# Kernel tuning notes

Hardware: AMD Instinct MI355X
Metric: run time of the kernel (lower is better)

## Reference

```python
import jax, jax.numpy as jnp
import numpy as np
import math

DIM = 512
HEADS = 8          # dim // num_head_channels = 512 // 64
HEAD_CH = 64
GROUPS = 32        # guided-diffusion normalization() = GroupNorm(32, dim)
EPS = 1e-5
CROSS_DIM = 768


def setup_inputs() -> dict:
    key = jax.random.key(0)
    ks = jax.random.split(key, 8)
    B, C, Hs, Ws, L = 16, DIM, 32, 32, 77
    x = jax.random.normal(ks[0], (B, C, Hs, Ws), dtype=jnp.float32)
    c = jax.random.normal(ks[1], (B, CROSS_DIM, L), dtype=jnp.float32)
    # GroupNorm affine params
    gamma = jnp.ones((C,), jnp.float32)
    beta = jnp.zeros((C,), jnp.float32)
    # 1x1 conv weights stored as [out, in]
    w_qkv = jax.random.normal(ks[2], (3 * C, C), jnp.float32) / math.sqrt(C)
    b_qkv = jnp.zeros((3 * C,), jnp.float32)
    w_c = jax.random.normal(ks[3], (2 * C, CROSS_DIM), jnp.float32) / math.sqrt(CROSS_DIM)
    b_c = jnp.zeros((2 * C,), jnp.float32)
    # NOTE: original proj_out is zero-initialized (zero_module); we use small
    # random weights so the reference exercises non-trivial math end-to-end.
    w_p = jax.random.normal(ks[4], (C, C), jnp.float32) / math.sqrt(C)
    b_p = jnp.zeros((C,), jnp.float32)
    return {"x": x, "c": c, "gamma": gamma, "beta": beta,
            "w_qkv": w_qkv, "b_qkv": b_qkv, "w_c": w_c, "b_c": b_c,
            "w_p": w_p, "b_p": b_p}


def reference(x, c, gamma, beta, w_qkv, b_qkv, w_c, b_c, w_p, b_p):
    B, C, Hs, Ws = x.shape
    T = Hs * Ws
    xf = x.reshape(B, C, T)

    # GroupNorm(32) over (channels_per_group, spatial)
    xg = xf.reshape(B, GROUPS, C // GROUPS, T)
    mean = xg.mean(axis=(2, 3), keepdims=True)
    var = xg.var(axis=(2, 3), keepdims=True)
    xn = ((xg - mean) * jax.lax.rsqrt(var + EPS)).reshape(B, C, T)
    xn = xn * gamma[None, :, None] + beta[None, :, None]

    # qkv 1x1 conv: [B, 3C, T]
    qkv = jnp.einsum('oc,bct->bot', w_qkv, xn) + b_qkv[None, :, None]
    q, k, v = jnp.split(qkv, 3, axis=1)
    q = q.reshape(B, HEADS, HEAD_CH, T)
    k = k.reshape(B, HEADS, HEAD_CH, T)
    v = v.reshape(B, HEADS, HEAD_CH, T)

    # cross-attn cond kv: [B, 2C, L] -> concat on sequence axis
    ckv = jnp.einsum('oc,bcl->bol', w_c, c) + b_c[None, :, None]
    kc, vc = jnp.split(ckv, 2, axis=1)
    L = c.shape[-1]
    k = jnp.concatenate([k, kc.reshape(B, HEADS, HEAD_CH, L)], axis=-1)
    v = jnp.concatenate([v, vc.reshape(B, HEADS, HEAD_CH, L)], axis=-1)

    scale = 1.0 / math.sqrt(HEAD_CH)
    # scores [B, H, T, T+L]; scale applied inside softmax as in FusedSoftmaxMaybeApex
    logits = jnp.einsum('bhct,bhcs->bhts', q, k) * scale
    w = jax.nn.softmax(logits, axis=-1)
    a = jnp.einsum('bhts,bhcs->bhct', w, v).reshape(B, C, T)

    h = jnp.einsum('oc,bct->bot', w_p, a) + b_p[None, :, None]
    return (xf + h).reshape(B, C, Hs, Ws)
```

## Files before the change

### kernel.cpp

```cpp
#include <hip/hip_runtime.h>

#define B_   16
#define C_   512
#define T_   1024
#define H_   8
#define D_   64
#define G_   32
#define L_   77
#define S_   1101
#define SPAD 1152
#define NPAD 51
#define CD_  768
#define BT_  (B_*T_)
#define SROW 72
#define QSC  0.18033688011112042f

typedef __bf16 bf16x8 __attribute__((ext_vector_type(8)));
typedef float  f32x4  __attribute__((ext_vector_type(4)));

static __device__ __forceinline__ unsigned short f2bf(float f) {
    unsigned int u = __float_as_uint(f);
    u = (u + 0x7fffu + ((u >> 16) & 1u)) >> 16;
    return (unsigned short)u;
}

static __device__ __forceinline__ unsigned int pk_bf16(float a, float b) {
    unsigned int d;
    asm("v_cvt_pk_bf16_f32 %0, %1, %2" : "=v"(d) : "v"(a), "v"(b));
    return d;
}

static __device__ __forceinline__ void gload_lds16(const unsigned short* g,
                                                   unsigned short* l) {
    __builtin_amdgcn_global_load_lds(
        (const __attribute__((address_space(1))) unsigned int*)g,
        (__attribute__((address_space(3))) unsigned int*)l, 16, 0, 0);
}

__global__ __launch_bounds__(256) void prep_k(const float* __restrict__ x,
                                              float* __restrict__ stats,
                                              const float* __restrict__ w_qkv,
                                              const float* __restrict__ w_p,
                                              const float* __restrict__ w_c,
                                              const float* __restrict__ cin,
                                              unsigned short* __restrict__ wqkv_pk,
                                              unsigned short* __restrict__ wp_pk,
                                              unsigned short* __restrict__ wc_pk,
                                              unsigned short* __restrict__ cpk) {
    const int tid = threadIdx.x;
    if (blockIdx.x < 512) {
        const int bg = blockIdx.x;
        const float* p = x + (size_t)bg * 16384;
        float s = 0.f, s2 = 0.f;
        for (int i = tid; i < 16384; i += 256) {
            float v = p[i];
            s += v; s2 += v * v;
        }
        __shared__ float rs[256], rs2[256];
        rs[tid] = s; rs2[tid] = s2;
        __syncthreads();
        for (int off = 128; off > 0; off >>= 1) {
            if (tid < off) { rs[tid] += rs[tid + off]; rs2[tid] += rs2[tid + off]; }
            __syncthreads();
        }
        if (tid == 0) {
            float mean = rs[0] * (1.0f / 16384.0f);
            float var  = rs2[0] * (1.0f / 16384.0f) - mean * mean;
            stats[2 * bg]     = mean;
            stats[2 * bg + 1] = rsqrtf(var + 1e-5f);
        }
        return;
    }
    if (blockIdx.x < 1408) {
        const int cid = (blockIdx.x - 512) * 256 + tid;
        const float* src;
        unsigned short* dst;
        if (cid < 98304) {
            const int ml = cid & 127, k8 = (cid >> 7) & 7, kt = (cid >> 10) & 7, mt = cid >> 13;
            src = w_qkv + (size_t)(mt * 128 + ml) * 512 + kt * 64 + k8 * 8;
            dst = wqkv_pk + (size_t)cid * 8;
        } else if (cid < 131072) {
            const int c2 = cid - 98304;
            const int ml = c2 & 127, k8 = (c2 >> 7) & 7, kt = (c2 >> 10) & 7, mt = c2 >> 13;
            src = w_p + (size_t)(mt * 128 + ml) * 512 + kt * 64 + k8 * 8;
            dst = wp_pk + (size_t)c2 * 8;
        } else {
            const int c3 = cid - 131072;
            const int ml = c3 & 127, k8 = (c3 >> 7) & 7;
            const int ktmt = c3 >> 10;
            const int kt = ktmt % 12, mt = ktmt / 12;
            src = w_c + (size_t)(mt * 128 + ml) * 768 + kt * 64 + k8 * 8;
            dst = wc_pk + (size_t)c3 * 8;
        }
        const float4 v0 = *(const float4*)src, v1 = *(const float4*)(src + 4);
        unsigned short tmp[8];
        tmp[0] = f2bf(v0.x); tmp[1] = f2bf(v0.y); tmp[2] = f2bf(v0.z); tmp[3] = f2bf(v0.w);
        tmp[4] = f2bf(v1.x); tmp[5] = f2bf(v1.y); tmp[6] = f2bf(v1.z); tmp[7] = f2bf(v1.w);
        *(uint4*)dst = *(uint4*)tmp;
        return;
    }
    const int idx2 = blockIdx.x - 1408;
    const int kt = idx2 % 12, b = idx2 / 12;
#pragma unroll
    for (int it = 0; it < 4; it++) {
        const int idx = it * 256 + tid;
        const int k8 = idx >> 7, l = idx & 127;
        unsigned short tmp[8];
        const float* src = cin + ((size_t)b * CD_ + kt * 64 + k8 * 8) * L_ + l;
#pragma unroll
        for (int q = 0; q < 8; q++)
            tmp[q] = (l < L_) ? f2bf(src[(size_t)q * L_]) : (unsigned short)0;
        *(uint4*)&cpk[(size_t)b * 98304 + ((size_t)(kt * 8 + k8)) * 1024 + (size_t)l * 8] =
            *(uint4*)tmp;
    }
}

__global__ __launch_bounds__(256) void gn_apply_t(const float* __restrict__ x,
                                                  const float* __restrict__ stats,
                                                  const float* __restrict__ gamma,
                                                  const float* __restrict__ beta,
                                                  unsigned short* __restrict__ xnT) {
    const int t0 = blockIdx.x * 64, kt = blockIdx.y, b = blockIdx.z;
    const int c0 = kt * 64;
    const int tid = threadIdx.x;
    __shared__ float st[64][66];
#pragma unroll
    for (int it = 0; it < 4; it++) {
        const int fid = it * 256 + tid;
        const int ci = fid >> 4, t4 = (fid & 15) * 4;
        const int c = c0 + ci;
        const float4 xv = *(const float4*)&x[((size_t)(b * C_ + c) << 10) + t0 + t4];
        const int bg = b * G_ + (c >> 4);
        const float mean = stats[2 * bg], istd = stats[2 * bg + 1];
        const float gs = gamma[c] * istd, gb = beta[c] - mean * gs;
        st[t4 + 0][ci] = xv.x * gs + gb;
        st[t4 + 1][ci] = xv.y * gs + gb;
        st[t4 + 2][ci] = xv.z * gs + gb;
        st[t4 + 3][ci] = xv.w * gs + gb;
    }
    __syncthreads();
#pragma unroll
    for (int it = 0; it < 2; it++) {
        const int cid = it * 256 + tid;
        const int k8 = cid >> 6, tl = cid & 63;
        const int n = (b << 10) + t0 + tl;
        const int nt = n >> 7, nm = n & 127;
        unsigned short tmp[8];
        const float* src = &st[tl][k8 * 8];
#pragma unroll
        for (int q = 0; q < 8; q++) tmp[q] = f2bf(src[q]);
        *(uint4*)&xnT[(((size_t)nt * 8 + kt) * 8 + k8) * 1024 + (size_t)nm * 8] = *(uint4*)tmp;
    }
}

template<int MODE, int KT>
__global__ __launch_bounds__(256) void mgemm_k(const unsigned short* __restrict__ Apk,
                                               const unsigned short* __restrict__ Bpk,
                                               const float* __restrict__ bias,
                                               const float* __restrict__ resid,
                                               unsigned short* __restrict__ qpk,
                                               unsigned short* __restrict__ kpk,
                                               unsigned short* __restrict__ vpk,
                                               float* __restrict__ outp) {
    __shared__ unsigned short lds[18432];
    const int tid = threadIdx.x, wave = tid >> 6, lane = tid & 63;
    const int quad = lane >> 4, l16 = lane & 15;
    const int nt = blockIdx.x, mt = blockIdx.y;
    const int mw = (wave & 1) * 64, nw = (wave >> 1) * 64;

    f32x4 acc[4][4];
#pragma unroll
    for (int i = 0; i < 4; i++)
#pragma unroll
        for (int j = 0; j < 4; j++) acc[i][j] = (f32x4){0.f, 0.f, 0.f, 0.f};

    const unsigned short* Ab = Apk + (size_t)mt * KT * 8192;
    const unsigned short* Bb = Bpk + ((MODE == 2) ? (size_t)blockIdx.z * KT * 8192 : 0)
                                   + (size_t)nt * KT * 8192;

    for (int kt = 0; kt < KT; kt++) {
        const unsigned short* as = Ab + kt * 8192 + wave * 2048 + lane * 8;
        const unsigned short* bs = Bb + kt * 8192 + wave * 2048 + lane * 8;
        unsigned short* la = lds + wave * 2048;
        unsigned short* lb = lds + 8192 + wave * 2048;
#pragma unroll
        for (int j = 0; j < 4; j++) {
            gload_lds16(as + j * 512, la + j * 512);
            gload_lds16(bs + j * 512, lb + j * 512);
        }
        __syncthreads();
#pragma unroll
        for (int kh = 0; kh < 2; kh++) {
            const int k8 = kh * 4 + quad;
            bf16x8 af[4], bfr[4];
#pragma unroll
            for (int i = 0; i < 4; i++) {
                af[i]  = *(const bf16x8*)&lds[(size_t)(k8 * 128 + mw + i * 16 + l16) * 8];
                bfr[i] = *(const bf16x8*)&lds[8192 + (size_t)(k8 * 128 + nw + i * 16 + l16) * 8];
            }
#pragma unroll
            for (int mi = 0; mi < 4; mi++)
#pragma unroll
                for (int ni = 0; ni < 4; ni++)
                    acc[mi][ni] = __builtin_amdgcn_mfma_f32_16x16x32_bf16(
                        af[mi], bfr[ni], acc[mi][ni], 0, 0, 0);
        }
        __syncthreads();
    }

    const int gm0 = mt * 128 + mw;
    const int gn0 = nt * 128 + nw;

    if (MODE == 1) {
        const int b = gn0 >> 10, t0 = gn0 & 1023;
#pragma unroll
        for (int mi = 0; mi < 4; mi++) {
#pragma unroll
            for (int r = 0; r < 4; r++) {
                const int m = gm0 + mi * 16 + quad * 4 + r;
                const float bv = bias[m];
                const size_t rowb = ((size_t)(b * C_ + m) << 10) + t0;
#pragma unroll
                for (int ni = 0; ni < 4; ni++) {
                    const size_t a = rowb + ni * 16 + l16;
                    outp[a] = acc[mi][ni][r] + bv + resid[a];
                }
            }
        }
        return;
    }

    const int region = gm0 >> 9;
    const int h = (gm0 & 511) >> 6;
    const int b = (MODE == 2) ? blockIdx.z : (gn0 >> 10);
    const int bh = b * 8 + h;
    const bool vregion = (MODE == 0) ? (region == 2) : (region == 1);

    if (!vregion) {
        const float sc = (MODE == 0 && region == 0) ? QSC : 1.0f;
        unsigned short* base;
        int trow0;
        size_t tilestride;
        if (MODE == 0) {
            base = (region == 0) ? qpk + (size_t)bh * 16 * 4096
                                 : kpk + (size_t)bh * 18 * 4096;
            trow0 = gn0 & 1023;
        } else {
            base = kpk + (size_t)(bh * 18 + 16 + (gn0 >> 6)) * 4096;
            trow0 = -1;
        }
        (void)tilestride;
#pragma unroll
        for (int mi = 0; mi < 4; mi++) {
            const int k8 = mi * 2 + (quad >> 1);
            const int sub = (quad & 1) * 4;
#pragma unroll
            for (int ni = 0; ni < 4; ni++) {
                float vv[4];
                bool valid = true;
                if (MODE == 2) valid = (gn0 + ni * 16 + l16) < L_;
#pragma unroll
                for (int r = 0; r < 4; r++)
                    vv[r] = valid ? (acc[mi][ni][r] + bias[gm0 + mi * 16 + quad * 4 + r]) * sc
                                  : 0.f;
                uint2 d;
                d.x = pk_bf16(vv[0], vv[1]);
                d.y = pk_bf16(vv[2], vv[3]);
                unsigned short* dst;
                if (MODE == 0) {
                    const int t = trow0 + ni * 16 + l16;
                    dst = base + (size_t)(t >> 6) * 4096 + ((size_t)k8 * 64 + (t & 63)) * 8 + sub;
                } else {
                    const int row = ni * 16 + l16;
                    dst = base + ((size_t)k8 * 64 + row) * 8 + sub;
                }
                *(uint2*)dst = d;
            }
        }
    } else {
        unsigned short* wlds = lds + wave * 4608;
#pragma unroll
        for (int mi = 0; mi < 4; mi++)
#pragma unroll
            for (int ni = 0; ni < 4; ni++) {
                bool valid = true;
                if (MODE == 2) valid = (gn0 + ni * 16 + l16) < L_;
#pragma unroll
                for (int r = 0; r < 4; r++) {
                    const float v = valid ? acc[mi][ni][r] + bias[gm0 + mi * 16 + quad * 4 + r]
                                          : 0.f;
                    wlds[(mi * 16 + quad * 4 + r) * SROW + ni * 16 + l16] = f2bf(v);
                }
            }
        __syncthreads();
        const int stile = (MODE == 0) ? ((gn0 & 1023) >> 6) : (16 + (gn0 >> 6));
        unsigned short* dst = vpk + (size_t)(bh * 18 + stile) * 4096;
        const int sk8 = lane & 7, cb = lane >> 3;
#pragma unroll
        for (int it = 0; it < 8; it++) {
            const int ch = it * 8 + cb;
            *(uint4*)&dst[((size_t)sk8 * 64 + ch) * 8] =
                *(const uint4*)&wlds[ch * SROW + sk8 * 8];
        }
    }
}

__global__ __launch_bounds__(256) void flash_k(const unsigned short* __restrict__ qpk,
                                               const unsigned short* __restrict__ kpk,
                                               const unsigned short* __restrict__ vpk,
                                               unsigned short* __restrict__ aT) {
    __shared__ __align__(16) unsigned short ks[4096];
    __shared__ __align__(16) unsigned short vs[4096];
    __shared__ __align__(16) unsigned short psA[4 * 16 * SROW];

    const int tid  = threadIdx.x;
    const int wave = tid >> 6, lane = tid & 63;
    const int quad = lane >> 4, l16 = lane & 15;
    const int bh  = blockIdx.x;
    const int b = bh >> 3, h = bh & 7;
    const int qt0 = blockIdx.y * 64;

    const unsigned short* qtb = qpk + ((size_t)bh * 16 + blockIdx.y) * 4096;
    const int qrow = wave * 16 + l16;
    const bf16x8 bq0 = *(const bf16x8*)&qtb[((size_t)quad * 64 + qrow) * 8];
    const bf16x8 bq1 = *(const bf16x8*)&qtb[((size_t)(quad + 4) * 64 + qrow) * 8];

    unsigned short* ps = psA + wave * 16 * SROW;

    float rsum = 0.f;
    f32x4 o_acc[4];
#pragma unroll
    for (int nb = 0; nb < 4; nb++) o_acc[nb] = (f32x4){0.f, 0.f, 0.f, 0.f};

    for (int stile = 0; stile < 18; stile++) {
        const unsigned short* kt = kpk + ((size_t)bh * 18 + stile) * 4096 + wave * 1024 + lane * 8;
        const unsigned short* vt = vpk + ((size_t)bh * 18 + stile) * 4096 + wave * 1024 + lane * 8;
        unsigned short* lk = ks + wave * 1024;
        unsigned short* lv = vs + wave * 1024;
        gload_lds16(kt, lk);       gload_lds16(kt + 512, lk + 512);
        gload_lds16(vt, lv);       gload_lds16(vt + 512, lv + 512);
        __syncthreads();

        f32x4 sacc[4];
#pragma unroll
        for (int sb = 0; sb < 4; sb++) {
            const bf16x8 ak0 = *(const bf16x8*)&ks[((size_t)quad * 64 + sb * 16 + l16) * 8];
            const bf16x8 ak1 = *(const bf16x8*)&ks[((size_t)(quad + 4) * 64 + sb * 16 + l16) * 8];
            f32x4 z = (f32x4){0.f, 0.f, 0.f, 0.f};
            z = __builtin_amdgcn_mfma_f32_16x16x32_bf16(ak0, bq0, z, 0, 0, 0);
            z = __builtin_amdgcn_mfma_f32_16x16x32_bf16(ak1, bq1, z, 0, 0, 0);
            sacc[sb] = z;
        }

#pragma unroll
        for (int sb = 0; sb < 4; sb++) {
            const float e0 = __builtin_exp2f(sacc[sb][0]);
            const float e1 = __builtin_exp2f(sacc[sb][1]);
            const float e2 = __builtin_exp2f(sacc[sb][2]);
            const float e3 = __builtin_exp2f(sacc[sb][3]);
            rsum += (e0 + e1) + (e2 + e3);
            uint2 d;
            d.x = pk_bf16(e0, e1);
            d.y = pk_bf16(e2, e3);
            *(uint2*)&ps[l16 * SROW + sb * 16 + quad * 4] = d;
        }
        asm volatile("s_waitcnt lgkmcnt(0)" ::: "memory");

        const bf16x8 ap0 = *(const bf16x8*)&ps[l16 * SROW + quad * 8];
        const bf16x8 ap1 = *(const bf16x8*)&ps[l16 * SROW + 32 + quad * 8];
#pragma unroll
        for (int nb = 0; nb < 4; nb++) {
            const bf16x8 bv0 = *(const bf16x8*)&vs[((size_t)quad * 64 + nb * 16 + l16) * 8];
            const bf16x8 bv1 = *(const bf16x8*)&vs[((size_t)(quad + 4) * 64 + nb * 16 + l16) * 8];
            o_acc[nb] = __builtin_amdgcn_mfma_f32_16x16x32_bf16(ap0, bv0, o_acc[nb], 0, 0, 0);
            o_acc[nb] = __builtin_amdgcn_mfma_f32_16x16x32_bf16(ap1, bv1, o_acc[nb], 0, 0, 0);
        }
        __syncthreads();
    }

    float lsum = rsum;
    lsum += __shfl_xor(lsum, 16);
    lsum += __shfl_xor(lsum, 32);
    float linv[4];
#pragma unroll
    for (int r = 0; r < 4; r++) {
        const float lr = __shfl(lsum, quad * 4 + r);
        linv[r] = 1.0f / (lr - (float)NPAD);
    }

#pragma unroll
    for (int nb = 0; nb < 4; nb++)
#pragma unroll
        for (int r = 0; r < 4; r++)
            ps[(quad * 4 + r) * SROW + nb * 16 + l16] = f2bf(o_acc[nb][r] * linv[r]);
    asm volatile("s_waitcnt lgkmcnt(0)" ::: "memory");
    const int k8 = lane >> 3;
#pragma unroll
    for (int it = 0; it < 2; it++) {
        const int tl = (lane & 7) + it * 8;
        const int n = (b << 10) + qt0 + wave * 16 + tl;
        const int ntb = n >> 7, nm = n & 127;
        *(uint4*)&aT[(((size_t)ntb * 8 + h) * 8 + k8) * 1024 + (size_t)nm * 8] =
            *(const uint4*)&ps[tl * SROW + k8 * 8];
    }
}

extern "C" void kernel_launch(void* const* d_in, const int* in_sizes, int n_in,
                              void* d_out, int out_size, void* d_ws, size_t ws_size,
                              hipStream_t stream) {
    const float* x     = (const float*)d_in[0];
    const float* cin   = (const float*)d_in[1];
    const float* gamma = (const float*)d_in[2];
    const float* beta  = (const float*)d_in[3];
    const float* w_qkv = (const float*)d_in[4];
    const float* b_qkv = (const float*)d_in[5];
    const float* w_c   = (const float*)d_in[6];
    const float* b_c   = (const float*)d_in[7];
    const float* w_p   = (const float*)d_in[8];
    const float* b_p   = (const float*)d_in[9];
    float* out = (float*)d_out;

    float* ws    = (float*)d_ws;
    float* stats = ws;
    unsigned short* xnT     = (unsigned short*)(ws + 1024);
    unsigned short* wqkv_pk = xnT + 8388608;
    unsigned short* wp_pk   = wqkv_pk + 786432;
    unsigned short* wc_pk   = wp_pk + 262144;
    unsigned short* cpk     = wc_pk + 786432;
    unsigned short* qpk     = cpk + 1572864;
    unsigned short* kpk     = qpk + 8388608;
    unsigned short* vpk     = kpk + 9437184;
    unsigned short* aT      = vpk + 9437184;

    prep_k<<<dim3(1600), 256, 0, stream>>>(x, stats, w_qkv, w_p, w_c, cin,
                                           wqkv_pk, wp_pk, wc_pk, cpk);
    gn_apply_t<<<dim3(16, 8, 16), 256, 0, stream>>>(x, stats, gamma, beta, xnT);
    mgemm_k<0, 8><<<dim3(128, 12), 256, 0, stream>>>(wqkv_pk, xnT, b_qkv, nullptr,
                                                     qpk, kpk, vpk, nullptr);
    mgemm_k<2, 12><<<dim3(1, 8, 16), 256, 0, stream>>>(wc_pk, cpk, b_c, nullptr,
                                                       nullptr, kpk, vpk, nullptr);
    flash_k<<<dim3(128, 16), 256, 0, stream>>>(qpk, kpk, vpk, aT);
    mgemm_k<1, 8><<<dim3(128, 4), 256, 0, stream>>>(wp_pk, aT, b_p, x,
                                                    nullptr, nullptr, nullptr, out);
}
```

Measured before the change: 277.2 us.

## Process two query sub-tiles per wave in flash attention to reuse K/V loads

Each wave of the flash attention kernel now handles 32 query rows (two 16-row sub-tiles) instead of 16, so a block covers 128 queries and the grid's y dimension halves. Each K and V tile staged in LDS, and the K/V fragments read from it, now feed twice as many MFMAs, cutting global K/V traffic and barrier count per query. The cost is higher register use, doubled P scratch in LDS and half as many blocks. A launch-bounds hint of 4 waves per SIMD is added to keep occupancy.

Measured after the change: 268.5 us. 3.1% less time.

```diff
diff --git a/kernel.cpp b/kernel.cpp
--- a/kernel.cpp
+++ b/kernel.cpp
@@ -305,32 +305,38 @@
     }
 }
 
-__global__ __launch_bounds__(256) void flash_k(const unsigned short* __restrict__ qpk,
-                                               const unsigned short* __restrict__ kpk,
-                                               const unsigned short* __restrict__ vpk,
-                                               unsigned short* __restrict__ aT) {
+__global__ __launch_bounds__(256, 4) void flash_k(const unsigned short* __restrict__ qpk,
+                                                  const unsigned short* __restrict__ kpk,
+                                                  const unsigned short* __restrict__ vpk,
+                                                  unsigned short* __restrict__ aT) {
     __shared__ __align__(16) unsigned short ks[4096];
     __shared__ __align__(16) unsigned short vs[4096];
-    __shared__ __align__(16) unsigned short psA[4 * 16 * SROW];
+    __shared__ __align__(16) unsigned short psA[4 * 32 * SROW];
 
     const int tid  = threadIdx.x;
     const int wave = tid >> 6, lane = tid & 63;
     const int quad = lane >> 4, l16 = lane & 15;
     const int bh  = blockIdx.x;
     const int b = bh >> 3, h = bh & 7;
-    const int qt0 = blockIdx.y * 64;
-
-    const unsigned short* qtb = qpk + ((size_t)bh * 16 + blockIdx.y) * 4096;
-    const int qrow = wave * 16 + l16;
-    const bf16x8 bq0 = *(const bf16x8*)&qtb[((size_t)quad * 64 + qrow) * 8];
-    const bf16x8 bq1 = *(const bf16x8*)&qtb[((size_t)(quad + 4) * 64 + qrow) * 8];
-
-    unsigned short* ps = psA + wave * 16 * SROW;
-
-    float rsum = 0.f;
-    f32x4 o_acc[4];
-#pragma unroll
-    for (int nb = 0; nb < 4; nb++) o_acc[nb] = (f32x4){0.f, 0.f, 0.f, 0.f};
+    const int qt0 = blockIdx.y * 128;
+
+    const unsigned short* qtb = qpk + ((size_t)bh * 16 + blockIdx.y * 2 + (wave >> 1)) * 4096;
+    const int qr0 = (wave & 1) * 32 + l16;
+    bf16x8 bq0[2], bq1[2];
+#pragma unroll
+    for (int s = 0; s < 2; s++) {
+        bq0[s] = *(const bf16x8*)&qtb[((size_t)quad * 64 + qr0 + s * 16) * 8];
+        bq1[s] = *(const bf16x8*)&qtb[((size_t)(quad + 4) * 64 + qr0 + s * 16) * 8];
+    }
+
+    unsigned short* ps = psA + wave * 32 * SROW;
+
+    float rsum[2] = {0.f, 0.f};
+    f32x4 o_acc[2][4];
+#pragma unroll
+    for (int s = 0; s < 2; s++)
+#pragma unroll
+        for (int nb = 0; nb < 4; nb++) o_acc[s][nb] = (f32x4){0.f, 0.f, 0.f, 0.f};
 
     for (int stile = 0; stile < 18; stile++) {
         const unsigned short* kt = kpk + ((size_t)bh * 18 + stile) * 4096 + wave * 1024 + lane * 8;
@@ -341,64 +347,83 @@
         gload_lds16(vt, lv);       gload_lds16(vt + 512, lv + 512);
         __syncthreads();
 
-        f32x4 sacc[4];
+        f32x4 sacc[2][4];
 #pragma unroll
         for (int sb = 0; sb < 4; sb++) {
             const bf16x8 ak0 = *(const bf16x8*)&ks[((size_t)quad * 64 + sb * 16 + l16) * 8];
             const bf16x8 ak1 = *(const bf16x8*)&ks[((size_t)(quad + 4) * 64 + sb * 16 + l16) * 8];
-            f32x4 z = (f32x4){0.f, 0.f, 0.f, 0.f};
-            z = __builtin_amdgcn_mfma_f32_16x16x32_bf16(ak0, bq0, z, 0, 0, 0);
-            z = __builtin_amdgcn_mfma_f32_16x16x32_bf16(ak1, bq1, z, 0, 0, 0);
-            sacc[sb] = z;
-        }
-
-#pragma unroll
-        for (int sb = 0; sb < 4; sb++) {
-            const float e0 = __builtin_exp2f(sacc[sb][0]);
-            const float e1 = __builtin_exp2f(sacc[sb][1]);
-            const float e2 = __builtin_exp2f(sacc[sb][2]);
-            const float e3 = __builtin_exp2f(sacc[sb][3]);
-            rsum += (e0 + e1) + (e2 + e3);
-            uint2 d;
-            d.x = pk_bf16(e0, e1);
-            d.y = pk_bf16(e2, e3);
-            *(uint2*)&ps[l16 * SROW + sb * 16 + quad * 4] = d;
+#pragma unroll
+            for (int s = 0; s < 2; s++) {
+                f32x4 z = (f32x4){0.f, 0.f, 0.f, 0.f};
+                z = __builtin_amdgcn_mfma_f32_16x16x32_bf16(ak0, bq0[s], z, 0, 0, 0);
+                z = __builtin_amdgcn_mfma_f32_16x16x32_bf16(ak1, bq1[s], z, 0, 0, 0);
+                sacc[s][sb] = z;
+            }
+        }
+
+#pragma unroll
+        for (int s = 0; s < 2; s++) {
+#pragma unroll
+            for (int sb = 0; sb < 4; sb++) {
+                const float e0 = __builtin_exp2f(sacc[s][sb][0]);
+                const float e1 = __builtin_exp2f(sacc[s][sb][1]);
+                const float e2 = __builtin_exp2f(sacc[s][sb][2]);
+                const float e3 = __builtin_exp2f(sacc[s][sb][3]);
+                rsum[s] += (e0 + e1) + (e2 + e3);
+                uint2 d;
+                d.x = pk_bf16(e0, e1);
+                d.y = pk_bf16(e2, e3);
+                *(uint2*)&ps[(s * 16 + l16) * SROW + sb * 16 + quad * 4] = d;
+            }
         }
         asm volatile("s_waitcnt lgkmcnt(0)" ::: "memory");
 
-        const bf16x8 ap0 = *(const bf16x8*)&ps[l16 * SROW + quad * 8];
-        const bf16x8 ap1 = *(const bf16x8*)&ps[l16 * SROW + 32 + quad * 8];
+        bf16x8 ap0[2], ap1[2];
+#pragma unroll
+        for (int s = 0; s < 2; s++) {
+            ap0[s] = *(const bf16x8*)&ps[(s * 16 + l16) * SROW + quad * 8];
+            ap1[s] = *(const bf16x8*)&ps[(s * 16 + l16) * SROW + 32 + quad * 8];
+        }
 #pragma unroll
         for (int nb = 0; nb < 4; nb++) {
             const bf16x8 bv0 = *(const bf16x8*)&vs[((size_t)quad * 64 + nb * 16 + l16) * 8];
             const bf16x8 bv1 = *(const bf16x8*)&vs[((size_t)(quad + 4) * 64 + nb * 16 + l16) * 8];
-            o_acc[nb] = __builtin_amdgcn_mfma_f32_16x16x32_bf16(ap0, bv0, o_acc[nb], 0, 0, 0);
-            o_acc[nb] = __builtin_amdgcn_mfma_f32_16x16x32_bf16(ap1, bv1, o_acc[nb], 0, 0, 0);
-        }
-        __syncthreads();
-    }
-
-    float lsum = rsum;
-    lsum += __shfl_xor(lsum, 16);
-    lsum += __shfl_xor(lsum, 32);
-    float linv[4];
-#pragma unroll
-    for (int r = 0; r < 4; r++) {
-        const float lr = __shfl(lsum, quad * 4 + r);
-        linv[r] = 1.0f / (lr - (float)NPAD);
-    }
-
-#pragma unroll
-    for (int nb = 0; nb < 4; nb++)
-#pragma unroll
-        for (int r = 0; r < 4; r++)
-            ps[(quad * 4 + r) * SROW + nb * 16 + l16] = f2bf(o_acc[nb][r] * linv[r]);
+#pragma unroll
+            for (int s = 0; s < 2; s++) {
+                o_acc[s][nb] = __builtin_amdgcn_mfma_f32_16x16x32_bf16(ap0[s], bv0, o_acc[s][nb], 0, 0, 0);
+                o_acc[s][nb] = __builtin_amdgcn_mfma_f32_16x16x32_bf16(ap1[s], bv1, o_acc[s][nb], 0, 0, 0);
+            }
+        }
+        __syncthreads();
+    }
+
+    float linv[2][4];
+#pragma unroll
+    for (int s = 0; s < 2; s++) {
+        float lsum = rsum[s];
+        lsum += __shfl_xor(lsum, 16);
+        lsum += __shfl_xor(lsum, 32);
+#pragma unroll
+        for (int r = 0; r < 4; r++) {
+            const float lr = __shfl(lsum, quad * 4 + r);
+            linv[s][r] = 1.0f / (lr - (float)NPAD);
+        }
+    }
+
+#pragma unroll
+    for (int s = 0; s < 2; s++)
+#pragma unroll
+        for (int nb = 0; nb < 4; nb++)
+#pragma unroll
+            for (int r = 0; r < 4; r++)
+                ps[(s * 16 + quad * 4 + r) * SROW + nb * 16 + l16] =
+                    f2bf(o_acc[s][nb][r] * linv[s][r]);
     asm volatile("s_waitcnt lgkmcnt(0)" ::: "memory");
     const int k8 = lane >> 3;
 #pragma unroll
-    for (int it = 0; it < 2; it++) {
+    for (int it = 0; it < 4; it++) {
         const int tl = (lane & 7) + it * 8;
-        const int n = (b << 10) + qt0 + wave * 16 + tl;
+        const int n = (b << 10) + qt0 + wave * 32 + tl;
         const int ntb = n >> 7, nm = n & 127;
         *(uint4*)&aT[(((size_t)ntb * 8 + h) * 8 + k8) * 1024 + (size_t)nm * 8] =
             *(const uint4*)&ps[tl * SROW + k8 * 8];
@@ -439,7 +464,7 @@
                                                      qpk, kpk, vpk, nullptr);
     mgemm_k<2, 12><<<dim3(1, 8, 16), 256, 0, stream>>>(wc_pk, cpk, b_c, nullptr,
                                                        nullptr, kpk, vpk, nullptr);
-    flash_k<<<dim3(128, 16), 256, 0, stream>>>(qpk, kpk, vpk, aT);
+    flash_k<<<dim3(128, 8), 256, 0, stream>>>(qpk, kpk, vpk, aT);
     mgemm_k<1, 8><<<dim3(128, 4), 256, 0, stream>>>(wp_pk, aT, b_p, x,
                                                     nullptr, nullptr, nullptr, out);
 }
```
